# Optimization experiments

Hardware: AMD Instinct MI355X
Metric: run time of the kernel (lower is better)

The kernel has to match this reference:

```python
import jax, jax.numpy as jnp
import numpy as np

N_NODES = 50000
N_EDGES = 800000
IN_NF = 128
HID = 128
OUT_NF = 128
EDGE_D = 16
EDGE_IN = 2 * IN_NF + 1 + EDGE_D + HID  # source, target, radial, edge_attr, prompt
NODE_IN = 2 * HID + IN_NF               # x, agg, prompt


def _lin(key, fan_in, fan_out, scale=None):
    s = scale if scale is not None else 1.0 / np.sqrt(fan_in)
    return jax.random.normal(key, (fan_in, fan_out), dtype=jnp.float32) * s


def setup_inputs() -> dict:
    key = jax.random.key(0)
    ks = jax.random.split(key, 20)
    inp = {
        "h": jax.random.normal(ks[0], (N_NODES, IN_NF), dtype=jnp.float32),
        "edge_index": jax.random.randint(ks[1], (2, N_EDGES), 0, N_NODES, dtype=jnp.int64 if jax.config.jax_enable_x64 else jnp.int32),
        "coord": jax.random.normal(ks[2], (N_NODES, 3), dtype=jnp.float32),
        "edge_attr": jax.random.normal(ks[3], (N_EDGES, EDGE_D), dtype=jnp.float32),
        "prompt": jax.random.normal(ks[4], (1, HID), dtype=jnp.float32),
        # edge_mlp: Linear(EDGE_IN,HID) -> SiLU -> Linear(HID,HID) -> SiLU
        "e_w1": _lin(ks[5], EDGE_IN, HID), "e_b1": jnp.zeros((HID,), jnp.float32),
        "e_w2": _lin(ks[6], HID, HID), "e_b2": jnp.zeros((HID,), jnp.float32),
        # node_mlp: Linear(NODE_IN,HID) -> SiLU -> Linear(HID,OUT_NF) -> SiLU
        "n_w1": _lin(ks[7], NODE_IN, HID), "n_b1": jnp.zeros((HID,), jnp.float32),
        "n_w2": _lin(ks[8], HID, OUT_NF), "n_b2": jnp.zeros((OUT_NF,), jnp.float32),
        # acc_mlp_edge: Linear(2H,HID) -> SiLU -> Linear(HID,1,no bias, xavier gain 1e-3)
        "ae_w1": _lin(ks[9], 2 * HID, HID), "ae_b1": jnp.zeros((HID,), jnp.float32),
        "ae_w2": _lin(ks[10], HID, 1, scale=0.001 * np.sqrt(6.0 / (HID + 1))),
        # acc_mlp_point: same structure
        "ap_w1": _lin(ks[11], 2 * HID, HID), "ap_b1": jnp.zeros((HID,), jnp.float32),
        "ap_w2": _lin(ks[12], HID, 1, scale=0.001 * np.sqrt(6.0 / (HID + 1))),
    }
    return inp


def reference(h, edge_index, coord, edge_attr, prompt,
              e_w1, e_b1, e_w2, e_b2,
              n_w1, n_b1, n_w2, n_b2,
              ae_w1, ae_b1, ae_w2,
              ap_w1, ap_b1, ap_w2):
    silu = jax.nn.silu
    row, col = edge_index[0], edge_index[1]
    N = h.shape[0]
    E = row.shape[0]

    # coord2radial (normalize=False)
    coord_diff = coord[row] - coord[col]                    # [E,3]
    radial = jnp.sum(coord_diff ** 2, axis=1, keepdims=True)  # [E,1]

    p_e = jnp.broadcast_to(prompt, (E, prompt.shape[1]))
    p_n = jnp.broadcast_to(prompt, (N, prompt.shape[1]))

    # edge_model (attention=False)
    ef_in = jnp.concatenate([h[row], h[col], radial, edge_attr, p_e], axis=1)
    edge_feat = silu(silu(ef_in @ e_w1 + e_b1) @ e_w2 + e_b2)  # [E,H]

    # node_model (residual=True, node_attr=None, ave=1)
    agg = jax.ops.segment_sum(edge_feat, row, num_segments=N)  # [N,H]
    node_in = jnp.concatenate([h, agg, p_n], axis=1)
    h_out = h + silu(silu(node_in @ n_w1 + n_b1) @ n_w2 + n_b2)  # [N,OUT_NF]

    # get_acc (tanh=False, change_coord=True); uses the UPDATED h
    ef2 = jnp.concatenate([edge_feat, p_e], axis=1)            # [E,2H]
    norm = jnp.maximum(jnp.linalg.norm(coord_diff, axis=1, keepdims=True), 1e-12)
    trans = (coord_diff / norm) * (silu(ef2 @ ae_w1 + ae_b1) @ ae_w2)  # [E,3]
    agg_c = jax.ops.segment_sum(trans, row, num_segments=N)    # [N,3]
    h_cat = jnp.concatenate([h_out, p_n], axis=1)              # [N,2H]
    acc = agg_c * (silu(h_cat @ ap_w1 + ap_b1) @ ap_w2)        # [N,3]

    return (h_out, coord, acc)
```

## Files before the change

### kernel.cpp

```cpp
#include <hip/hip_runtime.h>
#include <math.h>

#define NN 50000
#define NE 800000
#define HID 128

typedef __attribute__((ext_vector_type(8))) short short8;
typedef __attribute__((ext_vector_type(4))) float f32x4;

#define MFMA(a, b, c) __builtin_amdgcn_mfma_f32_16x16x32_bf16(a, b, c, 0, 0, 0)

__device__ __forceinline__ float silu_(float x) {
    return x / (1.0f + __expf(-x));
}

__device__ __forceinline__ short f2bf(float f) {
    union { float f; unsigned u; } v;
    v.f = f;
    unsigned r = v.u + 0x7fffu + ((v.u >> 16) & 1u);
    return (short)(r >> 16);
}

__device__ __forceinline__ short8 pack8(float4 lo, float4 hi) {
    short8 v;
    v[0] = f2bf(lo.x); v[1] = f2bf(lo.y); v[2] = f2bf(lo.z); v[3] = f2bf(lo.w);
    v[4] = f2bf(hi.x); v[5] = f2bf(hi.y); v[6] = f2bf(hi.z); v[7] = f2bf(hi.w);
    return v;
}

__device__ __forceinline__ void atom_pk_bf16(short* p, unsigned pk) {
    asm volatile("global_atomic_pk_add_bf16 %0, %1, off"
                 :: "v"(p), "v"(pk) : "memory");
}

__global__ __launch_bounds__(256) void conv_bf16(
    const float* __restrict__ in, short* __restrict__ out, int n8)
{
    const int i = blockIdx.x * 256 + threadIdx.x;
    if (i < n8) {
        const float4 lo = *(const float4*)(in + (size_t)i * 8);
        const float4 hi = *(const float4*)(in + (size_t)i * 8 + 4);
        *(short8*)(out + (size_t)i * 8) = pack8(lo, hi);
    }
}

__global__ __launch_bounds__(128) void pre_kernel(
    const float* __restrict__ prompt,
    const float* __restrict__ e_w1, const float* __restrict__ e_b1,
    const float* __restrict__ n_w1, const float* __restrict__ n_b1,
    const float* __restrict__ ae_w1, const float* __restrict__ ae_b1,
    const float* __restrict__ ap_w1, const float* __restrict__ ap_b1,
    float* __restrict__ pre)
{
    const int j = threadIdx.x;
    __shared__ float p[HID];
    p[j] = prompt[j];
    __syncthreads();
    float a0 = e_b1[j], a1 = n_b1[j], a2 = ae_b1[j], a3 = ap_b1[j];
    for (int k = 0; k < HID; ++k) {
        const float pk = p[k];
        a0 = fmaf(pk, e_w1[(273 + k) * HID + j], a0);
        a1 = fmaf(pk, n_w1[(256 + k) * HID + j], a1);
        a2 = fmaf(pk, ae_w1[(128 + k) * HID + j], a2);
        a3 = fmaf(pk, ap_w1[(128 + k) * HID + j], a3);
    }
    pre[j] = a0;
    pre[HID + j] = a1;
    pre[2 * HID + j] = a2;
    pre[3 * HID + j] = a3;
}

__global__ __launch_bounds__(64) void prep_weights(
    const float* __restrict__ e_w1, const float* __restrict__ e_w2,
    const float* __restrict__ ae_w1, const float* __restrict__ n_w1,
    const float* __restrict__ n_w2, const float* __restrict__ ap_w1,
    short* __restrict__ wsw)
{
    const int fid = blockIdx.x;
    const int l = threadIdx.x;
    int kt, nt;
    const float* W = nullptr;
    int kmax = 128;
    int e1 = 0;
    if (fid < 72) { kt = fid >> 3; nt = fid & 7; e1 = 1; }
    else if (fid < 104) { int f = fid - 72;  kt = f >> 3; nt = f & 7; W = e_w2; }
    else if (fid < 136) { int f = fid - 104; kt = f >> 3; nt = f & 7; W = ae_w1; }
    else if (fid < 200) { int f = fid - 136; kt = f >> 3; nt = f & 7; W = n_w1; kmax = 256; }
    else if (fid < 232) { int f = fid - 200; kt = f >> 3; nt = f & 7; W = n_w2; }
    else                { int f = fid - 232; kt = f >> 3; nt = f & 7; W = ap_w1; }

    short8 v;
#pragma unroll
    for (int i = 0; i < 8; ++i) {
        const int k = kt * 32 + ((l >> 4) * 8) + i;
        const int n = nt * 16 + (l & 15);
        float f = 0.0f;
        if (e1) {
            if (k < 256) f = e_w1[k * HID + n];
            else if (k < 272) f = e_w1[(k + 1) * HID + n];
            else if (k == 272) f = e_w1[256 * HID + n];
        } else {
            if (k < kmax) f = W[k * HID + n];
        }
        v[i] = f2bf(f);
    }
    *(short8*)&wsw[(size_t)fid * 512 + l * 8] = v;
}

__global__ __launch_bounds__(128, 3) void edge_kernel(
    const short* __restrict__ hb, const int* __restrict__ ei,
    const float* __restrict__ coord, const short* __restrict__ eb,
    const short* __restrict__ Bw1, const short* __restrict__ Bw2,
    const short* __restrict__ Bae,
    const float* __restrict__ e_b2, const float* __restrict__ ae_w2,
    const float* __restrict__ pre,
    short* __restrict__ agg, float* __restrict__ agg_c)
{
    const int t = threadIdx.x;
    const int wv = t >> 6, l = t & 63;
    const int lq = l >> 4, lr = l & 15;
    const int e0 = blockIdx.x * 64 + wv * 32;

    __shared__ __align__(16) short s_buf[2][32 * HID];
    char* Hb = (char*)&s_buf[wv][0];

    int r_row = 0, r_col = 0;
    float rad = 0.f, cnx = 0.f, cny = 0.f, cnz = 0.f;
    if (l < 32) {
        const int e = e0 + l;
        r_row = ei[e];
        r_col = ei[NE + e];
        const float dx = coord[r_row * 3 + 0] - coord[r_col * 3 + 0];
        const float dy = coord[r_row * 3 + 1] - coord[r_col * 3 + 1];
        const float dz = coord[r_row * 3 + 2] - coord[r_col * 3 + 2];
        rad = dx * dx + dy * dy + dz * dz;
        const float inv = 1.0f / fmaxf(sqrtf(rad), 1e-12f);
        cnx = dx * inv; cny = dy * inv; cnz = dz * inv;
    }

    short8 A[2][9];
#pragma unroll
    for (int mt = 0; mt < 2; ++mt) {
        const int me = mt * 16 + lr;
        const int srow = __shfl(r_row, me);
        const int scol = __shfl(r_col, me);
        const float radm = __shfl(rad, me);
#pragma unroll
        for (int kt = 0; kt < 8; ++kt) {
            const short* p = hb + (unsigned)(kt < 4 ? srow : scol) * HID
                                + (kt & 3) * 32 + lq * 8;
            A[mt][kt] = *(const short8*)p;
        }
        short8 v = {0, 0, 0, 0, 0, 0, 0, 0};
        if (lq < 2) {
            v = *(const short8*)(eb + (size_t)(e0 + me) * 16 + lq * 8);
        } else if (lq == 2) {
            v[0] = f2bf(radm);
        }
        A[mt][8] = v;
    }

    f32x4 acc[2][8];
#pragma unroll
    for (int tt = 0; tt < 8; ++tt) {
        const float pe = pre[tt * 16 + lr];
        acc[0][tt] = (f32x4){pe, pe, pe, pe};
        acc[1][tt] = acc[0][tt];
    }
#pragma unroll
    for (int kt = 0; kt < 9; ++kt) {
#pragma unroll
        for (int tt = 0; tt < 8; ++tt) {
            const short8 b = *(const short8*)&Bw1[((kt * 8 + tt) * 64 + l) * 8];
            acc[0][tt] = MFMA(A[0][kt], b, acc[0][tt]);
            acc[1][tt] = MFMA(A[1][kt], b, acc[1][tt]);
        }
    }
#pragma unroll
    for (int mt = 0; mt < 2; ++mt)
#pragma unroll
        for (int tt = 0; tt < 8; ++tt) {
            const int n = tt * 16 + lr;
#pragma unroll
            for (int r = 0; r < 4; ++r) {
                const int lm = mt * 16 + lq * 4 + r;
                const int off = (lm * 256 + n * 2) ^ ((lm & 7) << 4);
                *(short*)(Hb + off) = f2bf(silu_(acc[mt][tt][r]));
            }
        }
    asm volatile("s_waitcnt lgkmcnt(0)" ::: "memory");

    short8 A2[2][4];
#pragma unroll
    for (int mt = 0; mt < 2; ++mt) {
        const int lm = mt * 16 + lr;
        const int sw = (lm & 7) << 4;
#pragma unroll
        for (int kt = 0; kt < 4; ++kt)
            A2[mt][kt] = *(const short8*)(Hb + ((lm * 256 + kt * 64 + lq * 16) ^ sw));
    }
    f32x4 acc2[2][8];
#pragma unroll
    for (int tt = 0; tt < 8; ++tt) {
        const float b2 = e_b2[tt * 16 + lr];
        acc2[0][tt] = (f32x4){b2, b2, b2, b2};
        acc2[1][tt] = acc2[0][tt];
    }
#pragma unroll
    for (int kt = 0; kt < 4; ++kt) {
#pragma unroll
        for (int tt = 0; tt < 8; ++tt) {
            const short8 b = *(const short8*)&Bw2[((kt * 8 + tt) * 64 + l) * 8];
            acc2[0][tt] = MFMA(A2[0][kt], b, acc2[0][tt]);
            acc2[1][tt] = MFMA(A2[1][kt], b, acc2[1][tt]);
        }
    }

    int rowr[2][4];
#pragma unroll
    for (int mt = 0; mt < 2; ++mt)
#pragma unroll
        for (int r = 0; r < 4; ++r)
            rowr[mt][r] = __shfl(r_row, mt * 16 + lq * 4 + r);

#pragma unroll
    for (int mt = 0; mt < 2; ++mt)
#pragma unroll
        for (int tt = 0; tt < 8; ++tt) {
            const int n = tt * 16 + lr;
#pragma unroll
            for (int r = 0; r < 4; ++r) {
                const float v = silu_(acc2[mt][tt][r]);
                const int lm = mt * 16 + lq * 4 + r;
                const int off = (lm * 256 + n * 2) ^ ((lm & 7) << 4);
                const short vb = f2bf(v);
                *(short*)(Hb + off) = vb;
                const float vn = __shfl_xor(v, 1, 64);
                if ((lr & 1) == 0) {
                    const unsigned pk = (unsigned)(unsigned short)vb |
                                        ((unsigned)(unsigned short)f2bf(vn) << 16);
                    atom_pk_bf16(agg + (unsigned)rowr[mt][r] * HID + n, pk);
                }
            }
        }
    asm volatile("s_waitcnt lgkmcnt(0)" ::: "memory");

    short8 A3[2][4];
#pragma unroll
    for (int mt = 0; mt < 2; ++mt) {
        const int lm = mt * 16 + lr;
        const int sw = (lm & 7) << 4;
#pragma unroll
        for (int kt = 0; kt < 4; ++kt)
            A3[mt][kt] = *(const short8*)(Hb + ((lm * 256 + kt * 64 + lq * 16) ^ sw));
    }
    f32x4 acc3[2][8];
#pragma unroll
    for (int tt = 0; tt < 8; ++tt) {
        const float pa = pre[2 * HID + tt * 16 + lr];
        acc3[0][tt] = (f32x4){pa, pa, pa, pa};
        acc3[1][tt] = acc3[0][tt];
    }
#pragma unroll
    for (int kt = 0; kt < 4; ++kt) {
#pragma unroll
        for (int tt = 0; tt < 8; ++tt) {
            const short8 b = *(const short8*)&Bae[((kt * 8 + tt) * 64 + l) * 8];
            acc3[0][tt] = MFMA(A3[0][kt], b, acc3[0][tt]);
            acc3[1][tt] = MFMA(A3[1][kt], b, acc3[1][tt]);
        }
    }
    float w2v[8];
#pragma unroll
    for (int tt = 0; tt < 8; ++tt) w2v[tt] = ae_w2[tt * 16 + lr];

#pragma unroll
    for (int mt = 0; mt < 2; ++mt) {
        float p0 = 0.f, p1 = 0.f, p2 = 0.f, p3 = 0.f;
#pragma unroll
        for (int tt = 0; tt < 8; ++tt) {
            p0 += silu_(acc3[mt][tt][0]) * w2v[tt];
            p1 += silu_(acc3[mt][tt][1]) * w2v[tt];
            p2 += silu_(acc3[mt][tt][2]) * w2v[tt];
            p3 += silu_(acc3[mt][tt][3]) * w2v[tt];
        }
#pragma unroll
        for (int r = 0; r < 4; ++r) {
            float s = (r == 0) ? p0 : (r == 1) ? p1 : (r == 2) ? p2 : p3;
            s += __shfl_xor(s, 1, 16);
            s += __shfl_xor(s, 2, 16);
            s += __shfl_xor(s, 4, 16);
            s += __shfl_xor(s, 8, 16);
            const int lm = mt * 16 + lq * 4 + r;
            const float sx = __shfl(cnx, lm);
            const float sy = __shfl(cny, lm);
            const float sz = __shfl(cnz, lm);
            if (lr < 3) {
                const float cv = (lr == 0) ? sx : (lr == 1) ? sy : sz;
                atomicAdd(&agg_c[(unsigned)rowr[mt][r] * 3 + lr], cv * s);
            }
        }
    }
}

__global__ __launch_bounds__(128, 3) void node_kernel(
    const float* __restrict__ h, const short* __restrict__ hb,
    const float* __restrict__ coord,
    const short* __restrict__ Bn1, const short* __restrict__ Bn2,
    const short* __restrict__ Bap,
    const float* __restrict__ n_b2, const float* __restrict__ ap_w2,
    const float* __restrict__ pre,
    const short* __restrict__ agg,
    const float* __restrict__ agg_c,
    float* __restrict__ out_h, float* __restrict__ out_coord,
    float* __restrict__ out_acc)
{
    const int t = threadIdx.x;
    const int wv = t >> 6, l = t & 63;
    const int lq = l >> 4, lr = l & 15;
    const int n0 = blockIdx.x * 64 + wv * 32;

    __shared__ __align__(16) short s_buf[2][32 * HID];
    char* Hb = (char*)&s_buf[wv][0];

    short8 A[2][8];
#pragma unroll
    for (int mt = 0; mt < 2; ++mt) {
        int node = n0 + mt * 16 + lr;
        if (node >= NN) node = NN - 1;
#pragma unroll
        for (int kt = 0; kt < 4; ++kt)
            A[mt][kt] = *(const short8*)(hb + (unsigned)node * HID + kt * 32 + lq * 8);
#pragma unroll
        for (int kt = 4; kt < 8; ++kt)
            A[mt][kt] = *(const short8*)(agg + (unsigned)node * HID + (kt - 4) * 32 + lq * 8);
    }

    f32x4 acc[2][8];
#pragma unroll
    for (int tt = 0; tt < 8; ++tt) {
        const float pn = pre[HID + tt * 16 + lr];
        acc[0][tt] = (f32x4){pn, pn, pn, pn};
        acc[1][tt] = acc[0][tt];
    }
#pragma unroll
    for (int kt = 0; kt < 8; ++kt) {
#pragma unroll
        for (int tt = 0; tt < 8; ++tt) {
            const short8 b = *(const short8*)&Bn1[((kt * 8 + tt) * 64 + l) * 8];
            acc[0][tt] = MFMA(A[0][kt], b, acc[0][tt]);
            acc[1][tt] = MFMA(A[1][kt], b, acc[1][tt]);
        }
    }
#pragma unroll
    for (int mt = 0; mt < 2; ++mt)
#pragma unroll
        for (int tt = 0; tt < 8; ++tt) {
            const int n = tt * 16 + lr;
#pragma unroll
            for (int r = 0; r < 4; ++r) {
                const int lm = mt * 16 + lq * 4 + r;
                const int off = (lm * 256 + n * 2) ^ ((lm & 7) << 4);
                *(short*)(Hb + off) = f2bf(silu_(acc[mt][tt][r]));
            }
        }
    asm volatile("s_waitcnt lgkmcnt(0)" ::: "memory");

    short8 A2[2][4];
#pragma unroll
    for (int mt = 0; mt < 2; ++mt) {
        const int lm = mt * 16 + lr;
        const int sw = (lm & 7) << 4;
#pragma unroll
        for (int kt = 0; kt < 4; ++kt)
            A2[mt][kt] = *(const short8*)(Hb + ((lm * 256 + kt * 64 + lq * 16) ^ sw));
    }
    f32x4 acc2[2][8];
#pragma unroll
    for (int tt = 0; tt < 8; ++tt) {
        const float b2 = n_b2[tt * 16 + lr];
        acc2[0][tt] = (f32x4){b2, b2, b2, b2};
        acc2[1][tt] = acc2[0][tt];
    }
#pragma unroll
    for (int kt = 0; kt < 4; ++kt) {
#pragma unroll
        for (int tt = 0; tt < 8; ++tt) {
            const short8 b = *(const short8*)&Bn2[((kt * 8 + tt) * 64 + l) * 8];
            acc2[0][tt] = MFMA(A2[0][kt], b, acc2[0][tt]);
            acc2[1][tt] = MFMA(A2[1][kt], b, acc2[1][tt]);
        }
    }
#pragma unroll
    for (int mt = 0; mt < 2; ++mt)
#pragma unroll
        for (int tt = 0; tt < 8; ++tt) {
            const int n = tt * 16 + lr;
#pragma unroll
            for (int r = 0; r < 4; ++r) {
                const int lm = mt * 16 + lq * 4 + r;
                const int nd = n0 + lm;
                const unsigned ndc = (nd < NN) ? nd : (NN - 1);
                const float hv = h[ndc * HID + n];
                const float ho = hv + silu_(acc2[mt][tt][r]);
                if (nd < NN) out_h[(unsigned)nd * HID + n] = ho;
                const int off = (lm * 256 + n * 2) ^ ((lm & 7) << 4);
                *(short*)(Hb + off) = f2bf(ho);
            }
        }
    asm volatile("s_waitcnt lgkmcnt(0)" ::: "memory");

    short8 A3[2][4];
#pragma unroll
    for (int mt = 0; mt < 2; ++mt) {
        const int lm = mt * 16 + lr;
        const int sw = (lm & 7) << 4;
#pragma unroll
        for (int kt = 0; kt < 4; ++kt)
            A3[mt][kt] = *(const short8*)(Hb + ((lm * 256 + kt * 64 + lq * 16) ^ sw));
    }
    f32x4 acc3[2][8];
#pragma unroll
    for (int tt = 0; tt < 8; ++tt) {
        const float pa = pre[3 * HID + tt * 16 + lr];
        acc3[0][tt] = (f32x4){pa, pa, pa, pa};
        acc3[1][tt] = acc3[0][tt];
    }
#pragma unroll
    for (int kt = 0; kt < 4; ++kt) {
#pragma unroll
        for (int tt = 0; tt < 8; ++tt) {
            const short8 b = *(const short8*)&Bap[((kt * 8 + tt) * 64 + l) * 8];
            acc3[0][tt] = MFMA(A3[0][kt], b, acc3[0][tt]);
            acc3[1][tt] = MFMA(A3[1][kt], b, acc3[1][tt]);
        }
    }
    float w2v[8];
#pragma unroll
    for (int tt = 0; tt < 8; ++tt) w2v[tt] = ap_w2[tt * 16 + lr];

#pragma unroll
    for (int mt = 0; mt < 2; ++mt) {
        float p0 = 0.f, p1 = 0.f, p2 = 0.f, p3 = 0.f;
#pragma unroll
        for (int tt = 0; tt < 8; ++tt) {
            p0 += silu_(acc3[mt][tt][0]) * w2v[tt];
            p1 += silu_(acc3[mt][tt][1]) * w2v[tt];
            p2 += silu_(acc3[mt][tt][2]) * w2v[tt];
            p3 += silu_(acc3[mt][tt][3]) * w2v[tt];
        }
#pragma unroll
        for (int r = 0; r < 4; ++r) {
            float s = (r == 0) ? p0 : (r == 1) ? p1 : (r == 2) ? p2 : p3;
            s += __shfl_xor(s, 1, 16);
            s += __shfl_xor(s, 2, 16);
            s += __shfl_xor(s, 4, 16);
            s += __shfl_xor(s, 8, 16);
            const int lm = mt * 16 + lq * 4 + r;
            const int nd = n0 + lm;
            if (lr < 3 && nd < NN) {
                out_acc[(unsigned)nd * 3 + lr] = agg_c[(unsigned)nd * 3 + lr] * s;
                out_coord[(unsigned)nd * 3 + lr] = coord[(unsigned)nd * 3 + lr];
            }
        }
    }
}

extern "C" void kernel_launch(void* const* d_in, const int* in_sizes, int n_in,
                              void* d_out, int out_size, void* d_ws, size_t ws_size,
                              hipStream_t stream)
{
    const float* h      = (const float*)d_in[0];
    const int*   ei     = (const int*)d_in[1];
    const float* coord  = (const float*)d_in[2];
    const float* eattr  = (const float*)d_in[3];
    const float* prompt = (const float*)d_in[4];
    const float* e_w1 = (const float*)d_in[5];
    const float* e_b1 = (const float*)d_in[6];
    const float* e_w2 = (const float*)d_in[7];
    const float* e_b2 = (const float*)d_in[8];
    const float* n_w1 = (const float*)d_in[9];
    const float* n_b1 = (const float*)d_in[10];
    const float* n_w2 = (const float*)d_in[11];
    const float* n_b2 = (const float*)d_in[12];
    const float* ae_w1 = (const float*)d_in[13];
    const float* ae_b1 = (const float*)d_in[14];
    const float* ae_w2 = (const float*)d_in[15];
    const float* ap_w1 = (const float*)d_in[16];
    const float* ap_b1 = (const float*)d_in[17];
    const float* ap_w2 = (const float*)d_in[18];

    float* out       = (float*)d_out;
    float* out_h     = out;
    float* out_coord = out + (size_t)NN * HID;
    float* out_acc   = out_coord + (size_t)NN * 3;

    float* agg_c = (float*)d_ws;
    float* pre   = agg_c + (size_t)NN * 3;
    short* wsw   = (short*)(pre + 512);
    short* aggb  = wsw + 264 * 512;
    short* hb    = aggb + (size_t)NN * HID;

    short* eb = (short*)out_h;

    const short* Bw1 = wsw;
    const short* Bw2 = wsw + 36864;
    const short* Bae = wsw + 53248;
    const short* Bn1 = wsw + 69632;
    const short* Bn2 = wsw + 102400;
    const short* Bap = wsw + 118784;

    hipMemsetAsync(aggb, 0, (size_t)NN * HID * sizeof(short), stream);
    hipMemsetAsync(agg_c, 0, (size_t)NN * 3 * sizeof(float), stream);

    pre_kernel<<<1, 128, 0, stream>>>(prompt, e_w1, e_b1, n_w1, n_b1,
                                      ae_w1, ae_b1, ap_w1, ap_b1, pre);
    prep_weights<<<264, 64, 0, stream>>>(e_w1, e_w2, ae_w1, n_w1, n_w2, ap_w1, wsw);
    conv_bf16<<<(NN * HID / 8 + 255) / 256, 256, 0, stream>>>(h, hb, NN * HID / 8);
    conv_bf16<<<(NE * 16 / 8 + 255) / 256, 256, 0, stream>>>(eattr, eb, NE * 16 / 8);

    edge_kernel<<<NE / 64, 128, 0, stream>>>(hb, ei, coord, eb,
                                             Bw1, Bw2, Bae, e_b2, ae_w2,
                                             pre, aggb, agg_c);
    node_kernel<<<(NN + 63) / 64, 128, 0, stream>>>(h, hb, coord, Bn1, Bn2, Bap,
                                                    n_b2, ap_w2, pre,
                                                    aggb, agg_c,
                                                    out_h, out_coord, out_acc);
}
```

Before: 803.2 us.

## Precompute per-node first-layer projections to shrink per-edge GEMM

The first edge-MLP layer is split algebraically: h[row]@W_src and h[col]@W_dst are computed once per node in a new prep_P kernel and stored as bf16 tables P1/P2. The edge kernel then gathers these projections and runs only the small edge_attr/radial K-tile as MFMA, adding the gathered terms before SiLU. This cuts per-edge MFMA work for layer one roughly ninefold. The cost is an extra node-level kernel, larger workspace, and an extra bf16 rounding of the partial sums, which may slightly change accuracy.

```diff
diff --git a/kernel.cpp b/kernel.cpp
--- a/kernel.cpp
+++ b/kernel.cpp
@@ -12,6 +12,12 @@
 
 __device__ __forceinline__ float silu_(float x) {
     return x / (1.0f + __expf(-x));
+}
+
+__device__ __forceinline__ float bf2f(short x) {
+    union { unsigned u; float f; } v;
+    v.u = ((unsigned)(unsigned short)x) << 16;
+    return v.f;
 }
 
 __device__ __forceinline__ short f2bf(float f) {
@@ -26,6 +32,14 @@
     v[0] = f2bf(lo.x); v[1] = f2bf(lo.y); v[2] = f2bf(lo.z); v[3] = f2bf(lo.w);
     v[4] = f2bf(hi.x); v[5] = f2bf(hi.y); v[6] = f2bf(hi.z); v[7] = f2bf(hi.w);
     return v;
+}
+
+__device__ __forceinline__ short8 fuse_silu(short8 e, short8 p1, short8 p2) {
+    short8 o;
+#pragma unroll
+    for (int i = 0; i < 8; ++i)
+        o[i] = f2bf(silu_(bf2f(e[i]) + bf2f(p1[i]) + bf2f(p2[i])));
+    return o;
 }
 
 __device__ __forceinline__ void atom_pk_bf16(short* p, unsigned pk) {
@@ -107,9 +121,61 @@
     *(short8*)&wsw[(size_t)fid * 512 + l * 8] = v;
 }
 
+__global__ __launch_bounds__(128, 3) void prep_P(
+    const short* __restrict__ hb, const short* __restrict__ Bw1,
+    short* __restrict__ P1, short* __restrict__ P2)
+{
+    const int t = threadIdx.x;
+    const int wv = t >> 6, l = t & 63;
+    const int lq = l >> 4, lr = l & 15;
+    const int n0 = blockIdx.x * 64 + wv * 32;
+
+    short8 A[2][4];
+#pragma unroll
+    for (int mt = 0; mt < 2; ++mt) {
+        int node = n0 + mt * 16 + lr;
+        if (node >= NN) node = NN - 1;
+#pragma unroll
+        for (int kt = 0; kt < 4; ++kt)
+            A[mt][kt] = *(const short8*)(hb + (unsigned)node * HID + kt * 32 + lq * 8);
+    }
+#pragma unroll
+    for (int half = 0; half < 2; ++half) {
+        short* dst = half ? P2 : P1;
+        f32x4 acc[2][8];
+#pragma unroll
+        for (int tt = 0; tt < 8; ++tt) {
+            acc[0][tt] = (f32x4){0.f, 0.f, 0.f, 0.f};
+            acc[1][tt] = acc[0][tt];
+        }
+#pragma unroll
+        for (int kt = 0; kt < 4; ++kt) {
+#pragma unroll
+            for (int tt = 0; tt < 8; ++tt) {
+                const short8 b = *(const short8*)&Bw1[(((half * 4 + kt) * 8 + tt) * 64 + l) * 8];
+                acc[0][tt] = MFMA(A[0][kt], b, acc[0][tt]);
+                acc[1][tt] = MFMA(A[1][kt], b, acc[1][tt]);
+            }
+        }
+#pragma unroll
+        for (int mt = 0; mt < 2; ++mt)
+#pragma unroll
+            for (int tt = 0; tt < 8; ++tt) {
+                const int n = tt * 16 + lr;
+#pragma unroll
+                for (int r = 0; r < 4; ++r) {
+                    const int node = n0 + mt * 16 + lq * 4 + r;
+                    if (node < NN)
+                        dst[(unsigned)node * HID + n] = f2bf(acc[mt][tt][r]);
+                }
+            }
+    }
+}
+
 __global__ __launch_bounds__(128, 3) void edge_kernel(
-    const short* __restrict__ hb, const int* __restrict__ ei,
-    const float* __restrict__ coord, const short* __restrict__ eb,
+    const short* __restrict__ P1, const short* __restrict__ P2,
+    const int* __restrict__ ei, const float* __restrict__ coord,
+    const short* __restrict__ eb,
     const short* __restrict__ Bw1, const short* __restrict__ Bw2,
     const short* __restrict__ Bae,
     const float* __restrict__ e_b2, const float* __restrict__ ae_w2,
@@ -138,7 +204,8 @@
         cnx = dx * inv; cny = dy * inv; cnz = dz * inv;
     }
 
-    short8 A[2][9];
+    short8 p1f[2][4], p2f[2][4];
+    short8 Ae[2];
 #pragma unroll
     for (int mt = 0; mt < 2; ++mt) {
         const int me = mt * 16 + lr;
@@ -146,10 +213,9 @@
         const int scol = __shfl(r_col, me);
         const float radm = __shfl(rad, me);
 #pragma unroll
-        for (int kt = 0; kt < 8; ++kt) {
-            const short* p = hb + (unsigned)(kt < 4 ? srow : scol) * HID
-                                + (kt & 3) * 32 + lq * 8;
-            A[mt][kt] = *(const short8*)p;
+        for (int kt = 0; kt < 4; ++kt) {
+            p1f[mt][kt] = *(const short8*)(P1 + (unsigned)srow * HID + kt * 32 + lq * 8);
+            p2f[mt][kt] = *(const short8*)(P2 + (unsigned)scol * HID + kt * 32 + lq * 8);
         }
         short8 v = {0, 0, 0, 0, 0, 0, 0, 0};
         if (lq < 2) {
@@ -157,7 +223,7 @@
         } else if (lq == 2) {
             v[0] = f2bf(radm);
         }
-        A[mt][8] = v;
+        Ae[mt] = v;
     }
 
     f32x4 acc[2][8];
@@ -168,13 +234,10 @@
         acc[1][tt] = acc[0][tt];
     }
 #pragma unroll
-    for (int kt = 0; kt < 9; ++kt) {
-#pragma unroll
-        for (int tt = 0; tt < 8; ++tt) {
-            const short8 b = *(const short8*)&Bw1[((kt * 8 + tt) * 64 + l) * 8];
-            acc[0][tt] = MFMA(A[0][kt], b, acc[0][tt]);
-            acc[1][tt] = MFMA(A[1][kt], b, acc[1][tt]);
-        }
+    for (int tt = 0; tt < 8; ++tt) {
+        const short8 b = *(const short8*)&Bw1[((8 * 8 + tt) * 64 + l) * 8];
+        acc[0][tt] = MFMA(Ae[0], b, acc[0][tt]);
+        acc[1][tt] = MFMA(Ae[1], b, acc[1][tt]);
     }
 #pragma unroll
     for (int mt = 0; mt < 2; ++mt)
@@ -185,7 +248,7 @@
             for (int r = 0; r < 4; ++r) {
                 const int lm = mt * 16 + lq * 4 + r;
                 const int off = (lm * 256 + n * 2) ^ ((lm & 7) << 4);
-                *(short*)(Hb + off) = f2bf(silu_(acc[mt][tt][r]));
+                *(short*)(Hb + off) = f2bf(acc[mt][tt][r]);
             }
         }
     asm volatile("s_waitcnt lgkmcnt(0)" ::: "memory");
@@ -196,9 +259,12 @@
         const int lm = mt * 16 + lr;
         const int sw = (lm & 7) << 4;
 #pragma unroll
-        for (int kt = 0; kt < 4; ++kt)
-            A2[mt][kt] = *(const short8*)(Hb + ((lm * 256 + kt * 64 + lq * 16) ^ sw));
-    }
+        for (int kt = 0; kt < 4; ++kt) {
+            const short8 e = *(const short8*)(Hb + ((lm * 256 + kt * 64 + lq * 16) ^ sw));
+            A2[mt][kt] = fuse_silu(e, p1f[mt][kt], p2f[mt][kt]);
+        }
+    }
+
     f32x4 acc2[2][8];
 #pragma unroll
     for (int tt = 0; tt < 8; ++tt) {
@@ -500,6 +566,8 @@
     short* wsw   = (short*)(pre + 512);
     short* aggb  = wsw + 264 * 512;
     short* hb    = aggb + (size_t)NN * HID;
+    short* P1    = hb + (size_t)NN * HID;
+    short* P2    = P1 + (size_t)NN * HID;
 
     short* eb = (short*)out_h;
 
@@ -518,8 +586,9 @@
     prep_weights<<<264, 64, 0, stream>>>(e_w1, e_w2, ae_w1, n_w1, n_w2, ap_w1, wsw);
     conv_bf16<<<(NN * HID / 8 + 255) / 256, 256, 0, stream>>>(h, hb, NN * HID / 8);
     conv_bf16<<<(NE * 16 / 8 + 255) / 256, 256, 0, stream>>>(eattr, eb, NE * 16 / 8);
-
-    edge_kernel<<<NE / 64, 128, 0, stream>>>(hb, ei, coord, eb,
+    prep_P<<<(NN + 63) / 64, 128, 0, stream>>>(hb, Bw1, P1, P2);
+
+    edge_kernel<<<NE / 64, 128, 0, stream>>>(P1, P2, ei, coord, eb,
                                              Bw1, Bw2, Bae, e_b2, ae_w2,
                                              pre, aggb, agg_c);
     node_kernel<<<(NN + 63) / 64, 128, 0, stream>>>(h, hb, coord, Bn1, Bn2, Bap,
```

After: 827.0 us. +3.0%, slower.
